# Kernel optimization log

Measured on AMD Instinct MI355X. Metric: run time of the kernel, lower is better.

The kernel has to match this reference:

```python
import jax, jax.numpy as jnp
import numpy as np
from jax import lax

LEVEL = 128  # level_num

def _bn(x, g, b, m, v):
    # inference-mode BatchNorm, channel axis = 1
    sh = (1, -1) + (1,) * (x.ndim - 2)
    return (x - m.reshape(sh)) * (g.reshape(sh) * lax.rsqrt(v.reshape(sh) + 1e-5)) + b.reshape(sh)

def _leaky(a):
    return jnp.where(a > 0, a, 0.01 * a)

def _l2n(a):
    return a / jnp.maximum(jnp.linalg.norm(a, axis=1, keepdims=True), 1e-12)

def _resize_bilinear_ac(x, oh, ow):
    # bilinear, align_corners=True, NCHW
    n, c, h, w = x.shape
    ys = jnp.linspace(0.0, h - 1.0, oh)
    xs = jnp.linspace(0.0, w - 1.0, ow)
    y0 = jnp.floor(ys).astype(jnp.int32)
    x0 = jnp.floor(xs).astype(jnp.int32)
    y1 = jnp.minimum(y0 + 1, h - 1)
    x1 = jnp.minimum(x0 + 1, w - 1)
    wy = (ys - y0)[:, None]
    wx = (xs - x0)[None, :]
    Y0, Y1, X0, X1 = y0[:, None], y1[:, None], x0[None, :], x1[None, :]
    return (x[:, :, Y0, X0] * (1 - wy) * (1 - wx) + x[:, :, Y0, X1] * (1 - wy) * wx
            + x[:, :, Y1, X0] * wy * (1 - wx) + x[:, :, Y1, X1] * wy * wx)

def _forward(x, conv1_w, bn1_g, bn1_b, bn1_m, bn1_v, conv2_w, f1_w, f2_w, f2_g, f2_b, f2_m, f2_v,
             out1_w, out1_g, out1_b, out1_m, out1_v, k_w, q_w, v_w, out_w, out_g, out_b, out_m, out_v):
    # conv1: 3x3 conv + BN + LeakyReLU
    y = lax.conv_general_dilated(x, conv1_w, (1, 1), 'SAME', dimension_numbers=('NCHW', 'OIHW', 'NCHW'))
    y = _leaky(_bn(y, bn1_g, bn1_b, bn1_m, bn1_v))
    # conv2: 1x1 conv, 256->128
    x2 = jnp.einsum('nchw,oc->nohw', y, conv2_w)
    N, C, H, W = x2.shape  # C = 128
    x_ave = x2.mean(axis=(2, 3), keepdims=True)  # [N,C,1,1]
    cos = (_l2n(x_ave) * _l2n(x2)).sum(1)        # [N,H,W]
    sh, sw = H // 3, W // 3
    L = sh * sw
    # H,W divisible by 3 -> adaptive_avg_pool2d is identity
    cs = cos.reshape(N, 3, sh, 3, sw).transpose(0, 1, 3, 2, 4).reshape(N, 9, L).transpose(0, 2, 1)  # [N,L,9]
    # LBP bit packing vs center (index 4); weight 0 at index 4 (strict > gives 0 there)
    bits = (cs > cs[:, :, 4:5]).astype(x.dtype)
    wts = jnp.array([1, 2, 4, 8, 0, 16, 32, 64, 128], dtype=x.dtype)
    code = (bits * wts).sum(-1)  # [N,L]
    mn = code.min(-1, keepdims=True)
    mx = code.max(-1, keepdims=True)
    code = (code - mn) / (mx - mn)
    cmin = code.min(-1, keepdims=True)
    cmax = code.max(-1, keepdims=True)
    qlv = (2 * jnp.arange(LEVEL, dtype=x.dtype) + 1) / (2 * LEVEL) * (cmax - cmin) + cmin  # [N,LEVEL]
    inter = (qlv[:, 1] - qlv[:, 0])[:, None, None]  # [N,1,1]
    quant = 1 - jnp.abs(qlv[:, None, :] - code[:, :, None])  # [N,L,LEVEL]
    quant = jnp.where(quant > 1 - inter, quant, 0.0)
    sta = quant.sum(1)                                       # [N,LEVEL]
    sta = sta / sta.sum(-1, keepdims=True)
    sta2 = jnp.stack([qlv, sta], axis=1)                     # [N,2,LEVEL]
    h1 = _leaky(jnp.einsum('ncl,oc->nol', sta2, f1_w))       # f1: 2->64
    h2 = jax.nn.relu(_bn(jnp.einsum('ncl,oc->nol', h1, f2_w), f2_g, f2_b, f2_m, f2_v))  # f2: 64->128
    xa = jnp.broadcast_to(x_ave[:, :, 0, 0][:, :, None], (N, C, LEVEL))
    s = jnp.concatenate([h2, xa], axis=1)                    # [N,256,LEVEL]
    s = jax.nn.relu(_bn(jnp.einsum('ncl,oc->nol', s, out1_w), out1_g, out1_b, out1_m, out1_v))
    k = jnp.einsum('ncl,oc->nol', s, k_w)
    q = jnp.einsum('ncl,oc->nol', s, q_w)
    v = jnp.einsum('ncl,oc->nol', s, v_w)
    w = jax.nn.softmax(jnp.einsum('ncl,ncm->nlm', k, q), axis=-1)  # bmm(k^T, q)
    f = jnp.einsum('nlm,ncm->ncl', w, v)                            # bmm(w, v^T) then transpose
    f = jax.nn.relu(_bn(jnp.einsum('ncl,oc->nol', f, out_w), out_g, out_b, out_m, out_v))
    out = jnp.einsum('ncl,npl->ncp', f, quant).reshape(N, 256, sh, sh)  # bmm(f, quant^T)
    return _resize_bilinear_ac(out, H, W)

def setup_inputs() -> dict:
    key = jax.random.key(0)
    ks = jax.random.split(key, 16)
    f32 = jnp.float32
    def nrm(k, shape, s=0.05):
        return s * jax.random.normal(k, shape, f32)
    def bnp(k, c):
        k1, k2, k3, k4 = jax.random.split(k, 4)
        return (1.0 + 0.1 * jax.random.normal(k1, (c,), f32),
                0.1 * jax.random.normal(k2, (c,), f32),
                0.1 * jax.random.normal(k3, (c,), f32),
                jax.random.uniform(k4, (c,), f32, 0.5, 1.5))
    d = {}
    d['x'] = jax.random.normal(ks[0], (32, 512, 48, 48), f32)
    d['conv1_w'] = nrm(ks[1], (256, 512, 3, 3))
    d['bn1_g'], d['bn1_b'], d['bn1_m'], d['bn1_v'] = bnp(ks[2], 256)
    d['conv2_w'] = nrm(ks[3], (128, 256))
    d['f1_w'] = nrm(ks[4], (64, 2), 0.3)
    d['f2_w'] = nrm(ks[5], (128, 64), 0.1)
    d['f2_g'], d['f2_b'], d['f2_m'], d['f2_v'] = bnp(ks[6], 128)
    d['out1_w'] = nrm(ks[7], (256, 256))
    d['out1_g'], d['out1_b'], d['out1_m'], d['out1_v'] = bnp(ks[8], 256)
    d['k_w'] = nrm(ks[9], (256, 256))
    d['q_w'] = nrm(ks[10], (256, 256))
    d['v_w'] = nrm(ks[11], (256, 256))
    d['out_w'] = nrm(ks[12], (256, 256))
    d['out_g'], d['out_b'], d['out_m'], d['out_v'] = bnp(ks[13], 256)
    return d

def reference(x, conv1_w, bn1_g, bn1_b, bn1_m, bn1_v, conv2_w, f1_w, f2_w, f2_g, f2_b, f2_m, f2_v,
              out1_w, out1_g, out1_b, out1_m, out1_v, k_w, q_w, v_w, out_w, out_g, out_b, out_m, out_v):
    return _forward(x, conv1_w, bn1_g, bn1_b, bn1_m, bn1_v, conv2_w, f1_w, f2_w, f2_g, f2_b, f2_m, f2_v,
                    out1_w, out1_g, out1_b, out1_m, out1_v, k_w, q_w, v_w, out_w, out_g, out_b, out_m, out_v)
```

## Files before the change

kernel.cpp:

```cpp
#include <hip/hip_runtime.h>
#include <math.h>

#define N_IMG 32
#define P2304 2304
#define CIN 512
#define CMID 256
#define C2 128
#define LEV 128

typedef _Float16 half8 __attribute__((ext_vector_type(8)));
typedef float f32x16 __attribute__((ext_vector_type(16)));
typedef unsigned short u16;
typedef unsigned int u32;

__device__ __forceinline__ float wredSum(float v){
#pragma unroll
  for (int o = 32; o > 0; o >>= 1) v += __shfl_down(v, o, 64);
  return v;
}
__device__ __forceinline__ float wredMax(float v){
#pragma unroll
  for (int o = 32; o > 0; o >>= 1) v = fmaxf(v, __shfl_down(v, o, 64));
  return v;
}
__device__ __forceinline__ float wredMin(float v){
#pragma unroll
  for (int o = 32; o > 0; o >>= 1) v = fminf(v, __shfl_down(v, o, 64));
  return v;
}

__device__ __forceinline__ void gll16(const void* g, void* l){
  __builtin_amdgcn_global_load_lds(
      (const __attribute__((address_space(1))) void*)g,
      (__attribute__((address_space(3))) void*)l, 16, 0, 0);
}

__global__ void prep_w1_kernel(const float* __restrict__ w1,
                               uint4* __restrict__ Wh, uint4* __restrict__ Wl){
  int fid = blockIdx.x * 256 + threadIdx.x;
  int lam = fid & 63;
  int c32 = (fid >> 6) & 3;
  int cot = (fid >> 8) & 1;
  int kt  = fid >> 9;
  int co = cot * 128 + c32 * 32 + (lam & 31);
  half8 vh, vl;
#pragma unroll
  for (int j = 0; j < 8; ++j){
    int k = kt * 16 + ((lam >> 5) << 3) + j;
    int r = k >> 9;
    int ci = k & 511;
    float v = w1[co * (CIN * 9) + ci * 9 + r];
    _Float16 h = (_Float16)v;
    vh[j] = h;
    vl[j] = (_Float16)((v - (float)h) * 2048.0f);
  }
  Wh[fid] = *(uint4*)&vh;
  Wl[fid] = *(uint4*)&vl;
}

__global__ void prep_w2_kernel(const float* __restrict__ w2,
                               uint4* __restrict__ Wh, uint4* __restrict__ Wl){
  int fid = blockIdx.x * 256 + threadIdx.x;
  int lam = fid & 63;
  int c32 = (fid >> 6) & 3;
  int kt  = fid >> 8;
  int co = c32 * 32 + (lam & 31);
  half8 vh, vl;
#pragma unroll
  for (int j = 0; j < 8; ++j){
    int k = kt * 16 + ((lam >> 5) << 3) + j;
    float v = w2[co * CMID + k];
    _Float16 h = (_Float16)v;
    vh[j] = h;
    vl[j] = (_Float16)((v - (float)h) * 2048.0f);
  }
  Wh[fid] = *(uint4*)&vh;
  Wl[fid] = *(uint4*)&vl;
}

__global__ void prep_bn_kernel(const float* __restrict__ g1, const float* __restrict__ b1,
                               const float* __restrict__ m1, const float* __restrict__ v1,
                               float* __restrict__ s1, float* __restrict__ t1){
  int c = threadIdx.x;
  float s = g1[c] * (1.0f / sqrtf(v1[c] + 1e-5f));
  s1[c] = s;
  t1[c] = b1[c] - m1[c] * s;
}

__global__ void prep_x_kernel(const float* __restrict__ x,
                              u16* __restrict__ xh, u16* __restrict__ xl,
                              int n0){
  __shared__ float tile[128 * 49];
  const int t = threadIdx.x;
  const int b = blockIdx.x;
  const int n_loc = b / 50;
  const int hp = b - n_loc * 50;
  const int n = n0 + n_loc;
  const int h = hp - 1;
  const bool vrow = (h >= 0) && (h < 48);
  const size_t orow = ((size_t)n_loc * 50 + hp) * 50 * 512;
  for (int cc = 0; cc < 4; ++cc){
    if (vrow){
      const float* src = x + (((size_t)n * 512 + cc * 128) * 48 + h) * 48;
#pragma unroll
      for (int i = 0; i < 24; ++i){
        int idx = t + 256 * i;
        int w = idx % 48;
        int c = idx / 48;
        tile[c * 49 + w] = src[(size_t)c * 2304 + w];
      }
    }
    __syncthreads();
    for (int i = 0; i < 13; ++i){
      int idx = t + 256 * i;
      if (idx < 3200){
        int cpair = idx & 63;
        int wp = idx >> 6;
        int w = wp - 1;
        float v0 = 0.f, v1 = 0.f;
        if (vrow && (unsigned)w < 48u){
          v0 = tile[(cpair * 2) * 49 + w];
          v1 = tile[(cpair * 2 + 1) * 49 + w];
        }
        _Float16 h0 = (_Float16)v0, h1 = (_Float16)v1;
        _Float16 l0 = (_Float16)((v0 - (float)h0) * 2048.0f);
        _Float16 l1 = (_Float16)((v1 - (float)h1) * 2048.0f);
        union { _Float16 hh[2]; u32 uu; } ph, pl;
        ph.hh[0] = h0; ph.hh[1] = h1;
        pl.hh[0] = l0; pl.hh[1] = l1;
        ((u32*)(xh + orow + (size_t)wp * 512 + cc * 128))[cpair] = ph.uu;
        ((u32*)(xl + orow + (size_t)wp * 512 + cc * 128))[cpair] = pl.uu;
      }
    }
    __syncthreads();
  }
}

#define COMPUTE_M(CUR, KF)                                                    \
  {                                                                           \
    const int ct0 = (g & 1) * 2, pt0 = (g >> 1) * 2;                          \
    half8 fAh[2], fAl[2], fBh[2], fBl[2];                                     \
    _Pragma("unroll")                                                         \
    for (int a = 0; a < 2; ++a){                                              \
      fAh[a] = *(half8*)&Abuf[CUR][KF][0][(ct0 + a) * 512 + lam * 8];         \
      fAl[a] = *(half8*)&Abuf[CUR][KF][1][(ct0 + a) * 512 + lam * 8];         \
      fBh[a] = *(half8*)&Bbuf[CUR][KF][0][(pt0 + a) * 512 + lam * 8];         \
      fBl[a] = *(half8*)&Bbuf[CUR][KF][1][(pt0 + a) * 512 + lam * 8];         \
    }                                                                         \
    _Pragma("unroll")                                                         \
    for (int a = 0; a < 2; ++a)                                               \
      _Pragma("unroll")                                                       \
      for (int b = 0; b < 2; ++b){                                            \
        acc_hh[a][b] = __builtin_amdgcn_mfma_f32_32x32x16_f16(                \
            fAh[a], fBh[b], acc_hh[a][b], 0, 0, 0);                           \
        acc_x[a][b] = __builtin_amdgcn_mfma_f32_32x32x16_f16(                 \
            fAh[a], fBl[b], acc_x[a][b], 0, 0, 0);                            \
        acc_x[a][b] = __builtin_amdgcn_mfma_f32_32x32x16_f16(                 \
            fAl[a], fBh[b], acc_x[a][b], 0, 0, 0);                            \
      }                                                                       \
  }

#define WAITV16 asm volatile("s_waitcnt vmcnt(16)" ::: "memory")
#define WAITV8  asm volatile("s_waitcnt vmcnt(8)"  ::: "memory")
#define WAITV0  asm volatile("s_waitcnt vmcnt(0)"  ::: "memory")
#define BARSB { __builtin_amdgcn_s_barrier(); __builtin_amdgcn_sched_barrier(0); }

template<int NC>
__global__ __launch_bounds__(256, 2) void conv1_lds_kernel(
    const u16* __restrict__ xh, const u16* __restrict__ xl,
    const uint4* __restrict__ Wh, const uint4* __restrict__ Wl,
    const float* __restrict__ s1, const float* __restrict__ t1,
    u16* __restrict__ yh, u16* __restrict__ yl, int n0)
{
  __shared__ _Float16 Abuf[4][2][2][2048];
  __shared__ _Float16 Bbuf[4][2][2][2048];
  const int t = threadIdx.x;
  const int lam = t & 63;
  const int g = t >> 6;

  const int xcd = blockIdx.x & 7;
  const int rest = blockIdx.x >> 3;
  const int NPX = NC / 8;
  const int n_loc = xcd * NPX + rest / 36;
  const int inner = rest % 36;
  const int pt_blk = inner % 18;
  const int cot = inner / 18;
  const int n = n0 + n_loc;

  const int pbase = pt_blk * 128;
  const int khi = lam >> 5;
  const int pp = (g << 5) + (lam & 31);
  const int p = pbase + pp;
  const int ph = p / 48, pw = p - ph * 48;
  const u16* xh_n = xh + (size_t)n_loc * 1280000;
  const u16* xl_n = xl + (size_t)n_loc * 1280000;

  const int S = 144;

  f32x16 acc_hh[2][2], acc_x[2][2];
#pragma unroll
  for (int a = 0; a < 2; ++a)
#pragma unroll
    for (int b = 0; b < 2; ++b){
#pragma unroll
      for (int e = 0; e < 16; ++e){ acc_hh[a][b][e] = 0.f; acc_x[a][b][e] = 0.f; }
    }

#define ISSUE1(SV, BUF)                                                       \
  {                                                                           \
    int s_ = (SV);                                                            \
    int k0_ = 2 * s_;                                                         \
    _Pragma("unroll")                                                         \
    for (int kf = 0; kf < 2; ++kf){                                           \
      int fg_ = ((k0_ + kf) * 2 + cot) * 4 + g;                               \
      gll16(Wh + fg_ * 64 + lam, &Abuf[BUF][kf][0][t * 8]);                   \
      gll16(Wl + fg_ * 64 + lam, &Abuf[BUF][kf][1][t * 8]);                   \
    }                                                                         \
    int r_ = k0_ >> 5;                                          \
    int cb_ = (k0_ & 31) << 4;                       \
    int hh_ = ph + r_ / 3;                                    \
    int ww_ = pw + r_ % 3;                                    \
    const u16* sh_ = xh_n + ((hh_ * 50 + ww_) << 9) + cb_ + (khi << 3);       \
    const u16* sl_ = xl_n + ((hh_ * 50 + ww_) << 9) + cb_ + (khi << 3);       \
    _Pragma("unroll")                                                         \
    for (int kf = 0; kf < 2; ++kf){                                           \
      gll16(sh_ + kf * 16, &Bbuf[BUF][kf][0][t * 8]);                         \
      gll16(sl_ + kf * 16, &Bbuf[BUF][kf][1][t * 8]);                         \
    }                                                                         \
  }

  ISSUE1(0, 0);
  ISSUE1(1, 1);

  for (int s = 0; s < S - 2; ++s){
    ISSUE1(s + 2, (s + 2) & 3);
    WAITV16;
    BARSB;
    __builtin_amdgcn_s_setprio(1);
    COMPUTE_M(s & 3, 0);
    COMPUTE_M(s & 3, 1);
    __builtin_amdgcn_s_setprio(0);
  }
  WAITV8;
  BARSB;
  __builtin_amdgcn_s_setprio(1);
  COMPUTE_M((S - 2) & 3, 0);
  COMPUTE_M((S - 2) & 3, 1);
  __builtin_amdgcn_s_setprio(0);
  WAITV0;
  BARSB;
  __builtin_amdgcn_s_setprio(1);
  COMPUTE_M((S - 1) & 3, 0);
  COMPUTE_M((S - 1) & 3, 1);
  __builtin_amdgcn_s_setprio(0);
#undef ISSUE1

  const int cobase = cot * 128;
#pragma unroll
  for (int a = 0; a < 2; ++a){
    const int ctile = (g & 1) * 2 + a;
#pragma unroll
    for (int b = 0; b < 2; ++b){
      const int ptile = (g >> 1) * 2 + b;
      const int pg = pbase + ptile * 32 + (lam & 31);
      u16* dh = yh + (((size_t)n * P2304 + pg) << 8);
      u16* dl = yl + (((size_t)n * P2304 + pg) << 8);
#pragma unroll
      for (int q = 0; q < 4; ++q){
        const int co0 = cobase + ctile * 32 + 8 * q + 4 * khi;
        union { _Float16 h[4]; uint2 u; } Uh, Ul;
#pragma unroll
        for (int i = 0; i < 4; ++i){
          const int rg = 4 * q + i;
          const int co = co0 + i;
          float val = acc_hh[a][b][rg] + acc_x[a][b][rg] * (1.0f / 2048.0f);
          val = val * s1[co] + t1[co];
          val = val > 0.f ? val : 0.01f * val;
          _Float16 h = (_Float16)val;
          Uh.h[i] = h;
          Ul.h[i] = (_Float16)((val - (float)h) * 2048.0f);
        }
        *(uint2*)(dh + co0) = Uh.u;
        *(uint2*)(dl + co0) = Ul.u;
      }
    }
  }
}

__global__ __launch_bounds__(256, 2) void conv2_lds_kernel(
    const u16* __restrict__ yh, const u16* __restrict__ yl,
    const uint4* __restrict__ Wh, const uint4* __restrict__ Wl,
    float* __restrict__ out)
{
  __shared__ _Float16 Abuf[4][2][2][2048];
  __shared__ _Float16 Bbuf[4][2][2][2048];
  const int t = threadIdx.x;
  const int lam = t & 63;
  const int g = t >> 6;

  const int pt_blk = blockIdx.x % 18;
  const int n = blockIdx.x / 18;
  const int pbase = pt_blk * 128;
  const int khi = lam >> 5;
  const int p = pbase + (g << 5) + (lam & 31);
  const u16* yh_n = yh + (size_t)n * P2304 * 256;
  const u16* yl_n = yl + (size_t)n * P2304 * 256;

  const int S = 8;

  f32x16 acc_hh[2][2], acc_x[2][2];
#pragma unroll
  for (int a = 0; a < 2; ++a)
#pragma unroll
    for (int b = 0; b < 2; ++b){
#pragma unroll
      for (int e = 0; e < 16; ++e){ acc_hh[a][b][e] = 0.f; acc_x[a][b][e] = 0.f; }
    }

#define ISSUE2(SV, BUF)                                                       \
  {                                                                           \
    int s_ = (SV);                                                            \
    _Pragma("unroll")                                                         \
    for (int kf = 0; kf < 2; ++kf){                                           \
      int fg_ = (2 * s_ + kf) * 4 + g;                                        \
      gll16(Wh + fg_ * 64 + lam, &Abuf[BUF][kf][0][t * 8]);                   \
      gll16(Wl + fg_ * 64 + lam, &Abuf[BUF][kf][1][t * 8]);                   \
    }                                                                         \
    const u16* sh_ = yh_n + ((size_t)p << 8) + (s_ << 5) + (khi << 3);        \
    const u16* sl_ = yl_n + ((size_t)p << 8) + (s_ << 5) + (khi << 3);        \
    _Pragma("unroll")                                                         \
    for (int kf = 0; kf < 2; ++kf){                                           \
      gll16(sh_ + kf * 16, &Bbuf[BUF][kf][0][t * 8]);                         \
      gll16(sl_ + kf * 16, &Bbuf[BUF][kf][1][t * 8]);                         \
    }                                                                         \
  }

  ISSUE2(0, 0);
  ISSUE2(1, 1);

  for (int s = 0; s < S - 2; ++s){
    ISSUE2(s + 2, (s + 2) & 3);
    WAITV16;
    BARSB;
    __builtin_amdgcn_s_setprio(1);
    COMPUTE_M(s & 3, 0);
    COMPUTE_M(s & 3, 1);
    __builtin_amdgcn_s_setprio(0);
  }
  WAITV8;
  BARSB;
  __builtin_amdgcn_s_setprio(1);
  COMPUTE_M((S - 2) & 3, 0);
  COMPUTE_M((S - 2) & 3, 1);
  __builtin_amdgcn_s_setprio(0);
  WAITV0;
  BARSB;
  __builtin_amdgcn_s_setprio(1);
  COMPUTE_M((S - 1) & 3, 0);
  COMPUTE_M((S - 1) & 3, 1);
  __builtin_amdgcn_s_setprio(0);
#undef ISSUE2

#pragma unroll
  for (int a = 0; a < 2; ++a){
    const int ctile = (g & 1) * 2 + a;
#pragma unroll
    for (int b = 0; b < 2; ++b){
      const int ptile = (g >> 1) * 2 + b;
      const int pg = pbase + ptile * 32 + (lam & 31);
#pragma unroll
      for (int rg = 0; rg < 16; ++rg){
        const int row = (rg & 3) + 8 * (rg >> 2) + 4 * khi;
        const int co = ctile * 32 + row;
        float val = acc_hh[a][b][rg] + acc_x[a][b][rg] * (1.0f / 2048.0f);
        out[((size_t)n * C2 + co) * P2304 + pg] = val;
      }
    }
  }
}

template<int R, int CPT, int COTN, bool BN>
__global__ __launch_bounds__(256, 2) void conv_mfma_kernel(
    const float* __restrict__ in, const uint4* __restrict__ Wh, const uint4* __restrict__ Wl,
    const float* __restrict__ s1, const float* __restrict__ t1, float* __restrict__ out)
{
  __shared__ _Float16 Abuf[2][2][2][2048];
  __shared__ _Float16 Bbuf[2][2][2][2048];
  const int t = threadIdx.x;
  const int lam = t & 63;
  const int g = t >> 6;

  int n, pt_blk, cot;
  if (COTN == 2){
    int xcd = blockIdx.x & 7;
    int rest = blockIdx.x >> 3;
    n = xcd * 4 + rest / 36;
    int inner = rest % 36;
    pt_blk = inner % 18;
    cot = inner / 18;
  } else {
    pt_blk = blockIdx.x % 18;
    cot = 0;
    n = blockIdx.x / 18;
  }
  const int pbase = pt_blk * 128;
  const int cobase = cot * 128;

  const int khi = lam >> 5;
  const int pp = (g << 5) + (lam & 31);
  const int p = pbase + pp;
  const int ph = p / 48, pw = p - ph * 48;
  const float* in_n = in + (size_t)n * CPT * P2304;

  const int S = (R * CPT) / 32;
  const int KTPT = CPT / 16;

  f32x16 acc_hh[2][2], acc_x[2][2];
#pragma unroll
  for (int a = 0; a < 2; ++a)
#pragma unroll
    for (int b = 0; b < 2; ++b){
#pragma unroll
      for (int e = 0; e < 16; ++e){ acc_hh[a][b][e] = 0.f; acc_x[a][b][e] = 0.f; }
    }

  uint4 rAh[2], rAl[2];
  float rB[16];
  bool vmask;

#define ISSUE(SV)                                                             \
  {                                                                           \
    int s_ = (SV);                                                            \
    _Pragma("unroll")                                                         \
    for (int kf = 0; kf < 2; ++kf){                                           \
      int fi = (((2 * s_ + kf) * COTN + cot) * 4 + g) * 64 + lam;             \
      rAh[kf] = Wh[fi];                                                       \
      rAl[kf] = Wl[fi];                                                       \
    }                                                                         \
    int r_ = (R == 1) ? 0 : ((2 * s_) / KTPT);                                \
    int cbase_ = ((2 * s_) % KTPT) * 16;                                      \
    int dh_ = (R == 1) ? 0 : (r_ / 3 - 1);                                    \
    int dw_ = (R == 1) ? 0 : (r_ - (r_ / 3) * 3 - 1);                         \
    int hh_ = ph + dh_, ww_ = pw + dw_;                                       \
    vmask = ((unsigned)hh_ < 48u) & ((unsigned)ww_ < 48u);                    \
    int hc_ = min(max(hh_, 0), 47), wc_ = min(max(ww_, 0), 47);               \
    const float* src_ = in_n + hc_ * 48 + wc_                                 \
                        + (size_t)(cbase_ + khi * 8) * P2304;                 \
    _Pragma("unroll")                                                         \
    for (int kf = 0; kf < 2; ++kf)                                            \
      _Pragma("unroll")                                                       \
      for (int j = 0; j < 8; ++j)                                             \
        rB[kf * 8 + j] = src_[(kf * 16 + j) * P2304];                         \
  }

#define STASH(NXT)                                                            \
  {                                                                           \
    _Pragma("unroll")                                                         \
    for (int kf = 0; kf < 2; ++kf){                                           \
      *(uint4*)&Abuf[NXT][kf][0][t * 8] = rAh[kf];                            \
      *(uint4*)&Abuf[NXT][kf][1][t * 8] = rAl[kf];                            \
      half8 vh, vl;                                                           \
      _Pragma("unroll")                                                       \
      for (int j = 0; j < 8; ++j){                                            \
        float v = vmask ? rB[kf * 8 + j] : 0.0f;                              \
        _Float16 h = (_Float16)v;                                             \
        vh[j] = h;                                                            \
        vl[j] = (_Float16)((v - (float)h) * 2048.0f);                        \
      }                                                                       \
      *(half8*)&Bbuf[NXT][kf][0][t * 8] = vh;                                 \
      *(half8*)&Bbuf[NXT][kf][1][t * 8] = vl;                                 \
    }                                                                         \
  }

  ISSUE(0);
  STASH(0);
  __syncthreads();

  for (int s = 0; s < S; ++s){
    const int cur = s & 1, nxt = cur ^ 1;
    const bool more = (s + 1 < S);
    if (more) ISSUE(s + 1);
    COMPUTE_M(cur, 0);
    if (more) STASH(nxt);
    COMPUTE_M(cur, 1);
    __syncthreads();
  }
#undef ISSUE
#undef STASH

  const int M = COTN * 128;
#pragma unroll
  for (int a = 0; a < 2; ++a){
    const int ctile = (g & 1) * 2 + a;
#pragma unroll
    for (int b = 0; b < 2; ++b){
      const int ptile = (g >> 1) * 2 + b;
      const int pg = pbase + ptile * 32 + (lam & 31);
#pragma unroll
      for (int rg = 0; rg < 16; ++rg){
        const int row = (rg & 3) + 8 * (rg >> 2) + 4 * (lam >> 5);
        const int co = cobase + ctile * 32 + row;
        float val = acc_hh[a][b][rg] + acc_x[a][b][rg] * (1.0f / 2048.0f);
        if (BN){
          val = val * s1[co] + t1[co];
          val = val > 0.f ? val : 0.01f * val;
        }
        out[((size_t)n * M + co) * P2304 + pg] = val;
      }
    }
  }
}

__global__ void xave_kernel(const float* __restrict__ x2, float* __restrict__ xave){
  __shared__ float red[4];
  int nc = blockIdx.x, t = threadIdx.x;
  const float* row = x2 + nc * P2304;
  float s = 0.f;
#pragma unroll
  for (int i = 0; i < 9; i++) s += row[t + 256 * i];
  float w = wredSum(s);
  if ((t & 63) == 0) red[t >> 6] = w;
  __syncthreads();
  if (t == 0) xave[nc] = (red[0] + red[1] + red[2] + red[3]) * (1.0f / 2304.0f);
}

__global__ void xan_kernel(const float* __restrict__ xave, float* __restrict__ xan){
  __shared__ float red[2];
  int n = blockIdx.x, t = threadIdx.x;
  float v = xave[n * 128 + t];
  float w = wredSum(v * v);
  if ((t & 63) == 0) red[t >> 6] = w;
  __syncthreads();
  float norm = fmaxf(sqrtf(red[0] + red[1]), 1e-12f);
  xan[n * 128 + t] = v / norm;
}

__global__ void cos_kernel(const float* __restrict__ x2, const float* __restrict__ xan,
                           float* __restrict__ cosb){
  int idx = blockIdx.x * 256 + threadIdx.x;
  if (idx >= N_IMG * P2304) return;
  int n = idx / P2304;
  int p = idx - n * P2304;
  const float* xp = x2 + n * C2 * P2304 + p;
  const float* an = xan + n * 128;
  float dot = 0.f, ss = 0.f;
  for (int c = 0; c < 128; c++){
    float v = xp[c * P2304];
    dot += an[c] * v;
    ss  += v * v;
  }
  cosb[idx] = dot / fmaxf(sqrtf(ss), 1e-12f);
}

__global__ void lbp_kernel(const float* __restrict__ cosb, float* __restrict__ code,
                           float* __restrict__ qlv){
  __shared__ float red[4];
  int n = blockIdx.x;
  int l = threadIdx.x;
  int ir = l >> 4, ic = l & 15;
  const float* cn = cosb + n * P2304;
  float cs4 = cn[(16 + ir) * 48 + (16 + ic)];
  const float wts[9] = {1.f, 2.f, 4.f, 8.f, 0.f, 16.f, 32.f, 64.f, 128.f};
  float codev = 0.f;
#pragma unroll
  for (int j = 0; j < 9; j++){
    int jr = j / 3, jc = j - 3 * (j / 3);
    float vv = cn[(jr * 16 + ir) * 48 + (jc * 16 + ic)];
    if (vv > cs4) codev += wts[j];
  }
  float w;
  w = wredMin(codev);
  if ((l & 63) == 0) red[l >> 6] = w;
  __syncthreads();
  float mn = fminf(fminf(red[0], red[1]), fminf(red[2], red[3]));
  __syncthreads();
  w = wredMax(codev);
  if ((l & 63) == 0) red[l >> 6] = w;
  __syncthreads();
  float mx = fmaxf(fmaxf(red[0], red[1]), fmaxf(red[2], red[3]));
  __syncthreads();
  float cd = (codev - mn) / (mx - mn);
  w = wredMin(cd);
  if ((l & 63) == 0) red[l >> 6] = w;
  __syncthreads();
  float cmin = fminf(fminf(red[0], red[1]), fminf(red[2], red[3]));
  __syncthreads();
  w = wredMax(cd);
  if ((l & 63) == 0) red[l >> 6] = w;
  __syncthreads();
  float cmax = fmaxf(fmaxf(red[0], red[1]), fmaxf(red[2], red[3]));
  code[n * 256 + l] = cd;
  if (l < 128){
    float tmp = (float)(2 * l + 1) * (1.0f / 256.0f);
    qlv[n * 128 + l] = tmp * (cmax - cmin) + cmin;
  }
}

__global__ void quant_kernel(const float* __restrict__ code, const float* __restrict__ qlv,
                             float* __restrict__ quantT){
  __shared__ float cs[256];
  __shared__ float qs[128];
  int n = blockIdx.x, t = threadIdx.x;
  cs[t] = code[n * 256 + t];
  if (t < 128) qs[t] = qlv[n * 128 + t];
  __syncthreads();
  float thr = 1.0f - (qs[1] - qs[0]);
  float* dst = quantT + n * LEV * 256;
#pragma unroll 4
  for (int i = 0; i < 128; i++){
    int v = t + 256 * i;
    int lv = v >> 8;
    int p = v & 255;
    float qq = 1.0f - fabsf(qs[lv] - cs[p]);
    dst[v] = (qq > thr) ? qq : 0.f;
  }
}

__global__ void sta_kernel(const float* __restrict__ quantT, float* __restrict__ sta){
  __shared__ float red[2];
  int n = blockIdx.x, i = threadIdx.x;
  const float* qr = quantT + (n * LEV + i) * 256;
  float s = 0.f;
  for (int p = 0; p < 256; p++) s += qr[p];
  float w = wredSum(s);
  if ((i & 63) == 0) red[i >> 6] = w;
  __syncthreads();
  float tot = red[0] + red[1];
  sta[n * 128 + i] = s / tot;
}

__global__ void h1_kernel(const float* __restrict__ f1w, const float* __restrict__ qlv,
                          const float* __restrict__ sta, float* __restrict__ h1){
  int idx = blockIdx.x * 256 + threadIdx.x;
  if (idx >= N_IMG * 64 * 128) return;
  int l = idx & 127;
  int n = idx >> 13;
  int o = (idx >> 7) & 63;
  float a = f1w[o * 2] * qlv[n * 128 + l] + f1w[o * 2 + 1] * sta[n * 128 + l];
  h1[idx] = a > 0.f ? a : 0.01f * a;
}

__global__ void gemm_w_kernel(const float* __restrict__ Wm, const float* __restrict__ B,
                              float* __restrict__ Cout, int Cdim, int O, int total, int mode,
                              const float* __restrict__ g, const float* __restrict__ bb,
                              const float* __restrict__ mm, const float* __restrict__ vv){
  int idx = blockIdx.x * 256 + threadIdx.x;
  if (idx >= total) return;
  int per_n = (O >> 2) << 7;
  int n = idx / per_n;
  int rem = idx - n * per_n;
  int o0 = (rem >> 7) << 2;
  int l = rem & 127;
  const float* Bn = B + (n * Cdim) * 128 + l;
  const float* w0 = Wm + (o0 + 0) * Cdim;
  const float* w1 = Wm + (o0 + 1) * Cdim;
  const float* w2 = Wm + (o0 + 2) * Cdim;
  const float* w3 = Wm + (o0 + 3) * Cdim;
  float a0 = 0, a1 = 0, a2 = 0, a3 = 0;
  for (int c = 0; c < Cdim; c++){
    float bv = Bn[c * 128];
    a0 += w0[c] * bv; a1 += w1[c] * bv; a2 += w2[c] * bv; a3 += w3[c] * bv;
  }
  float av[4] = {a0, a1, a2, a3};
#pragma unroll
  for (int j = 0; j < 4; j++){
    int o = o0 + j;
    float val = av[j];
    if (mode == 1){
      float s = g[o] * (1.0f / sqrtf(vv[o] + 1e-5f));
      val = (val - mm[o]) * s + bb[o];
      val = fmaxf(val, 0.f);
    }
    Cout[(n * O + o) * 128 + l] = val;
  }
}

__global__ void concat_kernel(const float* __restrict__ h2, const float* __restrict__ xave,
                              float* __restrict__ s){
  int idx = blockIdx.x * 256 + threadIdx.x;
  if (idx >= N_IMG * 256 * 128) return;
  int l = idx & 127;
  int c = (idx >> 7) & 255;
  int n = idx >> 15;
  s[idx] = (c < 128) ? h2[(n * 128 + c) * 128 + l] : xave[n * 128 + (c - 128)];
}

__global__ void attn_sc_kernel(const float* __restrict__ k, const float* __restrict__ q,
                               float* __restrict__ sc){
  int idx = blockIdx.x * 256 + threadIdx.x;
  if (idx >= N_IMG * 32 * 128) return;
  int m = idx & 127;
  int l0 = ((idx >> 7) & 31) << 2;
  int n = idx >> 12;
  const float* kn = k + n * 256 * 128;
  const float* qn = q + n * 256 * 128 + m;
  float a0 = 0, a1 = 0, a2 = 0, a3 = 0;
  for (int c = 0; c < 256; c++){
    float qv = qn[c * 128];
    const float* kr = kn + c * 128 + l0;
    a0 += kr[0] * qv; a1 += kr[1] * qv; a2 += kr[2] * qv; a3 += kr[3] * qv;
  }
  float* dst = sc + (n * 128 + l0) * 128 + m;
  dst[0] = a0; dst[128] = a1; dst[256] = a2; dst[384] = a3;
}

__global__ void softmax_kernel(float* __restrict__ sc){
  __shared__ float red[2];
  int row = blockIdx.x;
  int t = threadIdx.x;
  float v = sc[row * 128 + t];
  float w = wredMax(v);
  if ((t & 63) == 0) red[t >> 6] = w;
  __syncthreads();
  float mx = fmaxf(red[0], red[1]);
  float e = expf(v - mx);
  float s = wredSum(e);
  __syncthreads();
  if ((t & 63) == 0) red[t >> 6] = s;
  __syncthreads();
  sc[row * 128 + t] = e / (red[0] + red[1]);
}

__global__ void transpose_sc_kernel(const float* __restrict__ sc, float* __restrict__ scT){
  int idx = blockIdx.x * 256 + threadIdx.x;
  if (idx >= N_IMG * 128 * 128) return;
  int l = idx & 127;
  int m = (idx >> 7) & 127;
  int n = idx >> 14;
  scT[idx] = sc[(n * 128 + l) * 128 + m];
}

__global__ void attn_f_kernel(const float* __restrict__ vb, const float* __restrict__ scT,
                              float* __restrict__ f){
  int idx = blockIdx.x * 256 + threadIdx.x;
  if (idx >= N_IMG * 64 * 128) return;
  int l = idx & 127;
  int c0 = ((idx >> 7) & 63) << 2;
  int n = idx >> 13;
  const float* vn = vb + (n * 256 + c0) * 128;
  const float* sn = scT + n * 128 * 128 + l;
  float a0 = 0, a1 = 0, a2 = 0, a3 = 0;
  for (int m = 0; m < 128; m++){
    float sv = sn[m * 128];
    a0 += vn[m] * sv; a1 += vn[128 + m] * sv; a2 += vn[256 + m] * sv; a3 += vn[384 + m] * sv;
  }
  float* dst = f + (n * 256 + c0) * 128 + l;
  dst[0] = a0; dst[128] = a1; dst[256] = a2; dst[384] = a3;
}

__global__ void final_kernel(const float* __restrict__ g, const float* __restrict__ quantT,
                             float* __restrict__ outs){
  int idx = blockIdx.x * 256 + threadIdx.x;
  if (idx >= N_IMG * 64 * 256) return;
  int p = idx & 255;
  int c0 = ((idx >> 8) & 63) << 2;
  int n = idx >> 14;
  const float* gn = g + (n * 256 + c0) * 128;
  const float* qn = quantT + (n * LEV) * 256 + p;
  float a0 = 0, a1 = 0, a2 = 0, a3 = 0;
  for (int lv = 0; lv < 128; lv++){
    float qv = qn[lv * 256];
    a0 += gn[lv] * qv; a1 += gn[128 + lv] * qv; a2 += gn[256 + lv] * qv; a3 += gn[384 + lv] * qv;
  }
  float* dst = outs + (n * 256 + c0) * 256 + p;
  dst[0] = a0; dst[256] = a1; dst[512] = a2; dst[768] = a3;
}

__global__ void resize_kernel(const float* __restrict__ outs, float* __restrict__ dout){
  int idx = blockIdx.x * 256 + threadIdx.x;
  if (idx >= N_IMG * 256 * P2304) return;
  int ow = idx % 48;
  int tmp = idx / 48;
  int oh = tmp % 48;
  int nc = tmp / 48;
  const float* src = outs + nc * 256;
  float fy = oh * (15.0f / 47.0f);
  float fx = ow * (15.0f / 47.0f);
  int y0 = (int)fy;
  int x0 = (int)fx;
  int y1 = min(y0 + 1, 15);
  int x1 = min(x0 + 1, 15);
  float wy = fy - (float)y0;
  float wx = fx - (float)x0;
  float v00 = src[y0 * 16 + x0], v01 = src[y0 * 16 + x1];
  float v10 = src[y1 * 16 + x0], v11 = src[y1 * 16 + x1];
  dout[idx] = v00 * (1.f - wy) * (1.f - wx) + v01 * (1.f - wy) * wx
            + v10 * wy * (1.f - wx) + v11 * wy * wx;
}

extern "C" void kernel_launch(void* const* d_in, const int* in_sizes, int n_in,
                              void* d_out, int out_size, void* d_ws, size_t ws_size,
                              hipStream_t stream)
{
  const float* x       = (const float*)d_in[0];
  const float* conv1_w = (const float*)d_in[1];
  const float* bn1_g   = (const float*)d_in[2];
  const float* bn1_b   = (const float*)d_in[3];
  const float* bn1_m   = (const float*)d_in[4];
  const float* bn1_v   = (const float*)d_in[5];
  const float* conv2_w = (const float*)d_in[6];
  const float* f1_w    = (const float*)d_in[7];
  const float* f2_w    = (const float*)d_in[8];
  const float* f2_g    = (const float*)d_in[9];
  const float* f2_b    = (const float*)d_in[10];
  const float* f2_m    = (const float*)d_in[11];
  const float* f2_v    = (const float*)d_in[12];
  const float* out1_w  = (const float*)d_in[13];
  const float* out1_g  = (const float*)d_in[14];
  const float* out1_b  = (const float*)d_in[15];
  const float* out1_m  = (const float*)d_in[16];
  const float* out1_v  = (const float*)d_in[17];
  const float* k_w     = (const float*)d_in[18];
  const float* q_w     = (const float*)d_in[19];
  const float* v_w     = (const float*)d_in[20];
  const float* out_w   = (const float*)d_in[21];
  const float* out_g   = (const float*)d_in[22];
  const float* out_b   = (const float*)d_in[23];
  const float* out_m   = (const float*)d_in[24];
  const float* out_v   = (const float*)d_in[25];

  float* ws = (float*)d_ws;
  float* dout = (float*)d_out;

  float* w_y   = ws;
  float* w_x2  = ws + 18874368;
  float* w_W1h = ws + 28311552;
  float* w_W1l = ws + 28901376;
  float* w_W2h = ws + 29491200;
  float* w_W2l = ws + 29507584;
  float* w_s1  = ws + 29523968;
  float* w_t1  = ws + 29524224;
  float* w_xave = w_y + 0;
  float* w_xan  = w_y + 4096;
  float* w_cos  = w_y + 8192;
  float* w_code = w_y + 81920;
  float* w_qlv  = w_y + 90112;
  float* w_sta  = w_y + 94208;
  float* w_quant= w_y + 98304;
  float* w_h1   = w_y + 1146880;
  float* w_h2   = w_y + 1409024;
  float* w_s    = w_y + 1933312;
  float* w_k    = w_y + 2981888;
  float* w_q    = w_y + 4030464;
  float* w_v    = w_y + 5079040;
  float* w_sc   = w_y + 6127616;
  float* w_scT  = w_y + 6651904;
  float* w_f    = w_y + 7176192;
  float* w_g    = w_y + 8224768;
  float* w_outs = w_y + 9273344;
  float* w_s2   = w_y + 11370496;

  prep_w1_kernel<<<576, 256, 0, stream>>>(conv1_w, (uint4*)w_W1h, (uint4*)w_W1l);
  prep_w2_kernel<<<16, 256, 0, stream>>>(conv2_w, (uint4*)w_W2h, (uint4*)w_W2l);
  prep_bn_kernel<<<1, 256, 0, stream>>>(bn1_g, bn1_b, bn1_m, bn1_v, w_s1, w_t1);

  const size_t BASE_F = 29524480;
  const size_t XPI_F  = 640000;
  const size_t ws_f = ws_size / 4;
  int NCc = 0;
  if (ws_f >= BASE_F + 2 * 32 * XPI_F)      NCc = 32;
  else if (ws_f >= BASE_F + 2 * 16 * XPI_F) NCc = 16;

  if (NCc > 0){
    u16* w_xh = (u16*)(ws + BASE_F);
    u16* w_xl = w_xh + (size_t)NCc * 1280000;
    u16* w_yh = (u16*)w_y;
    u16* w_yl = (u16*)(w_y + 9437184);
    const int nchunk = N_IMG / NCc;
    for (int c = 0; c < nchunk; ++c){
      int n0 = c * NCc;
      prep_x_kernel<<<NCc * 50, 256, 0, stream>>>(x, w_xh, w_xl, n0);
      if (NCc == 32)
        conv1_lds_kernel<32><<<1152, 256, 0, stream>>>(
            w_xh, w_xl, (const uint4*)w_W1h, (const uint4*)w_W1l, w_s1, w_t1,
            w_yh, w_yl, n0);
      else
        conv1_lds_kernel<16><<<576, 256, 0, stream>>>(
            w_xh, w_xl, (const uint4*)w_W1h, (const uint4*)w_W1l, w_s1, w_t1,
            w_yh, w_yl, n0);
    }
    conv2_lds_kernel<<<576, 256, 0, stream>>>(
        w_yh, w_yl, (const uint4*)w_W2h, (const uint4*)w_W2l, w_x2);
  } else {
    conv_mfma_kernel<9, 512, 2, true><<<1152, 256, 0, stream>>>(
        x, (const uint4*)w_W1h, (const uint4*)w_W1l, w_s1, w_t1, w_y);
    conv_mfma_kernel<1, 256, 1, false><<<576, 256, 0, stream>>>(
        w_y, (const uint4*)w_W2h, (const uint4*)w_W2l, w_s1, w_t1, w_x2);
  }

  xave_kernel<<<4096, 256, 0, stream>>>(w_x2, w_xave);
  xan_kernel<<<32, 128, 0, stream>>>(w_xave, w_xan);
  cos_kernel<<<288, 256, 0, stream>>>(w_x2, w_xan, w_cos);
  lbp_kernel<<<32, 256, 0, stream>>>(w_cos, w_code, w_qlv);
  quant_kernel<<<32, 256, 0, stream>>>(w_code, w_qlv, w_quant);
  sta_kernel<<<32, 128, 0, stream>>>(w_quant, w_sta);
  h1_kernel<<<1024, 256, 0, stream>>>(f1_w, w_qlv, w_sta, w_h1);
  gemm_w_kernel<<<512, 256, 0, stream>>>(f2_w, w_h1, w_h2, 64, 128, N_IMG * 32 * 128, 1,
                                         f2_g, f2_b, f2_m, f2_v);
  concat_kernel<<<4096, 256, 0, stream>>>(w_h2, w_xave, w_s);
  gemm_w_kernel<<<1024, 256, 0, stream>>>(out1_w, w_s, w_s2, 256, 256, N_IMG * 64 * 128, 1,
                                          out1_g, out1_b, out1_m, out1_v);
  gemm_w_kernel<<<1024, 256, 0, stream>>>(k_w, w_s2, w_k, 256, 256, N_IMG * 64 * 128, 0,
                                          nullptr, nullptr, nullptr, nullptr);
  gemm_w_kernel<<<1024, 256, 0, stream>>>(q_w, w_s2, w_q, 256, 256, N_IMG * 64 * 128, 0,
                                          nullptr, nullptr, nullptr, nullptr);
  gemm_w_kernel<<<1024, 256, 0, stream>>>(v_w, w_s2, w_v, 256, 256, N_IMG * 64 * 128, 0,
                                          nullptr, nullptr, nullptr, nullptr);
  attn_sc_kernel<<<512, 256, 0, stream>>>(w_k, w_q, w_sc);
  softmax_kernel<<<4096, 128, 0, stream>>>(w_sc);
  transpose_sc_kernel<<<2048, 256, 0, stream>>>(w_sc, w_scT);
  attn_f_kernel<<<1024, 256, 0, stream>>>(w_v, w_scT, w_f);
  gemm_w_kernel<<<1024, 256, 0, stream>>>(out_w, w_f, w_g, 256, 256, N_IMG * 64 * 128, 1,
                                          out_g, out_b, out_m, out_v);
  final_kernel<<<2048, 256, 0, stream>>>(w_g, w_quant, w_outs);
  resize_kernel<<<73728, 256, 0, stream>>>(w_outs, dout);
}
```

Measured before the change: 1.774 ms.

## Use channel-blocked 16-wide layout for padded input and conv1 output; double-buffer LDS

Changes the fp16 hi/lo staging layout of the padded input and of the conv1 activations from pixel-major with 512/256 contiguous channels to a channel-block-major layout with 16 channels per block. The conv1 and conv2 LDS pipelines drop from 4-deep to 2-deep buffering, and each refill is issued after an extra barrier once the current stage is consumed. Halving LDS may allow more resident blocks per CU, but the two-stage pipeline exposes more load latency and adds a barrier per step. The new layout also changes global access strides for the gather loads and the epilogue stores.

```diff
diff --git a/kernel.cpp b/kernel.cpp
--- a/kernel.cpp
+++ b/kernel.cpp
@@ -98,7 +98,7 @@
   const int n = n0 + n_loc;
   const int h = hp - 1;
   const bool vrow = (h >= 0) && (h < 48);
-  const size_t orow = ((size_t)n_loc * 50 + hp) * 50 * 512;
+  const size_t base_n = (size_t)n_loc * 1280000;
   for (int cc = 0; cc < 4; ++cc){
     if (vrow){
       const float* src = x + (((size_t)n * 512 + cc * 128) * 48 + h) * 48;
@@ -114,13 +114,16 @@
     for (int i = 0; i < 13; ++i){
       int idx = t + 256 * i;
       if (idx < 3200){
-        int cpair = idx & 63;
-        int wp = idx >> 6;
+        int ck_loc = idx / 400;
+        int rem = idx - ck_loc * 400;
+        int wp = rem >> 3;
+        int clp = rem & 7;
         int w = wp - 1;
+        int c_loc = ck_loc * 16 + clp * 2;
         float v0 = 0.f, v1 = 0.f;
         if (vrow && (unsigned)w < 48u){
-          v0 = tile[(cpair * 2) * 49 + w];
-          v1 = tile[(cpair * 2 + 1) * 49 + w];
+          v0 = tile[c_loc * 49 + w];
+          v1 = tile[(c_loc + 1) * 49 + w];
         }
         _Float16 h0 = (_Float16)v0, h1 = (_Float16)v1;
         _Float16 l0 = (_Float16)((v0 - (float)h0) * 2048.0f);
@@ -128,8 +131,10 @@
         union { _Float16 hh[2]; u32 uu; } ph, pl;
         ph.hh[0] = h0; ph.hh[1] = h1;
         pl.hh[0] = l0; pl.hh[1] = l1;
-        ((u32*)(xh + orow + (size_t)wp * 512 + cc * 128))[cpair] = ph.uu;
-        ((u32*)(xl + orow + (size_t)wp * 512 + cc * 128))[cpair] = pl.uu;
+        size_t off = base_n + ((size_t)(cc * 8 + ck_loc) * 2500
+                               + hp * 50 + wp) * 16 + clp * 2;
+        *(u32*)(xh + off) = ph.uu;
+        *(u32*)(xl + off) = pl.uu;
       }
     }
     __syncthreads();
@@ -160,7 +165,6 @@
       }                                                                       \
   }
 
-#define WAITV16 asm volatile("s_waitcnt vmcnt(16)" ::: "memory")
 #define WAITV8  asm volatile("s_waitcnt vmcnt(8)"  ::: "memory")
 #define WAITV0  asm volatile("s_waitcnt vmcnt(0)"  ::: "memory")
 #define BARSB { __builtin_amdgcn_s_barrier(); __builtin_amdgcn_sched_barrier(0); }
@@ -172,8 +176,8 @@
     const float* __restrict__ s1, const float* __restrict__ t1,
     u16* __restrict__ yh, u16* __restrict__ yl, int n0)
 {
-  __shared__ _Float16 Abuf[4][2][2][2048];
-  __shared__ _Float16 Bbuf[4][2][2][2048];
+  __shared__ _Float16 Abuf[2][2][2][2048];
+  __shared__ _Float16 Bbuf[2][2][2][2048];
   const int t = threadIdx.x;
   const int lam = t & 63;
   const int g = t >> 6;
@@ -217,41 +221,36 @@
       gll16(Wl + fg_ * 64 + lam, &Abuf[BUF][kf][1][t * 8]);                   \
     }                                                                         \
     int r_ = k0_ >> 5;                                          \
-    int cb_ = (k0_ & 31) << 4;                       \
-    int hh_ = ph + r_ / 3;                                    \
-    int ww_ = pw + r_ % 3;                                    \
-    const u16* sh_ = xh_n + ((hh_ * 50 + ww_) << 9) + cb_ + (khi << 3);       \
-    const u16* sl_ = xl_n + ((hh_ * 50 + ww_) << 9) + cb_ + (khi << 3);       \
+    int ck0_ = k0_ & 31;                         \
+    int qpp_ = (ph + r_ / 3) * 50 + (pw + r_ % 3);            \
     _Pragma("unroll")                                                         \
     for (int kf = 0; kf < 2; ++kf){                                           \
-      gll16(sh_ + kf * 16, &Bbuf[BUF][kf][0][t * 8]);                         \
-      gll16(sl_ + kf * 16, &Bbuf[BUF][kf][1][t * 8]);                         \
+      size_t o_ = ((size_t)(ck0_ + kf) * 2500 + qpp_) * 16 + (khi << 3);      \
+      gll16(xh_n + o_, &Bbuf[BUF][kf][0][t * 8]);                             \
+      gll16(xl_n + o_, &Bbuf[BUF][kf][1][t * 8]);                             \
     }                                                                         \
   }
 
   ISSUE1(0, 0);
   ISSUE1(1, 1);
 
-  for (int s = 0; s < S - 2; ++s){
-    ISSUE1(s + 2, (s + 2) & 3);
-    WAITV16;
+  for (int s = 0; s < S - 1; ++s){
+    WAITV8;
     BARSB;
     __builtin_amdgcn_s_setprio(1);
-    COMPUTE_M(s & 3, 0);
-    COMPUTE_M(s & 3, 1);
+    COMPUTE_M(s & 1, 0);
+    COMPUTE_M(s & 1, 1);
     __builtin_amdgcn_s_setprio(0);
-  }
-  WAITV8;
-  BARSB;
-  __builtin_amdgcn_s_setprio(1);
-  COMPUTE_M((S - 2) & 3, 0);
-  COMPUTE_M((S - 2) & 3, 1);
-  __builtin_amdgcn_s_setprio(0);
+    if (s + 2 < S){
+      BARSB;
+      ISSUE1(s + 2, s & 1);
+    }
+  }
   WAITV0;
   BARSB;
   __builtin_amdgcn_s_setprio(1);
-  COMPUTE_M((S - 1) & 3, 0);
-  COMPUTE_M((S - 1) & 3, 1);
+  COMPUTE_M((S - 1) & 1, 0);
+  COMPUTE_M((S - 1) & 1, 1);
   __builtin_amdgcn_s_setprio(0);
 #undef ISSUE1
 
@@ -263,11 +262,10 @@
     for (int b = 0; b < 2; ++b){
       const int ptile = (g >> 1) * 2 + b;
       const int pg = pbase + ptile * 32 + (lam & 31);
-      u16* dh = yh + (((size_t)n * P2304 + pg) << 8);
-      u16* dl = yl + (((size_t)n * P2304 + pg) << 8);
 #pragma unroll
       for (int q = 0; q < 4; ++q){
         const int co0 = cobase + ctile * 32 + 8 * q + 4 * khi;
+        const int co16 = co0 >> 4, col = co0 & 15;
         union { _Float16 h[4]; uint2 u; } Uh, Ul;
 #pragma unroll
         for (int i = 0; i < 4; ++i){
@@ -280,8 +278,9 @@
           Uh.h[i] = h;
           Ul.h[i] = (_Float16)((val - (float)h) * 2048.0f);
         }
-        *(uint2*)(dh + co0) = Uh.u;
-        *(uint2*)(dl + co0) = Ul.u;
+        size_t off = (((size_t)n * 16 + co16) * P2304 + pg) * 16 + col;
+        *(uint2*)(yh + off) = Uh.u;
+        *(uint2*)(yl + off) = Ul.u;
       }
     }
   }
@@ -292,8 +291,8 @@
     const uint4* __restrict__ Wh, const uint4* __restrict__ Wl,
     float* __restrict__ out)
 {
-  __shared__ _Float16 Abuf[4][2][2][2048];
-  __shared__ _Float16 Bbuf[4][2][2][2048];
+  __shared__ _Float16 Abuf[2][2][2][2048];
+  __shared__ _Float16 Bbuf[2][2][2][2048];
   const int t = threadIdx.x;
   const int lam = t & 63;
   const int g = t >> 6;
@@ -303,8 +302,8 @@
   const int pbase = pt_blk * 128;
   const int khi = lam >> 5;
   const int p = pbase + (g << 5) + (lam & 31);
-  const u16* yh_n = yh + (size_t)n * P2304 * 256;
-  const u16* yl_n = yl + (size_t)n * P2304 * 256;
+  const u16* yh_n = yh + (size_t)n * 589824;
+  const u16* yl_n = yl + (size_t)n * 589824;
 
   const int S = 8;
 
@@ -320,44 +319,41 @@
 #define ISSUE2(SV, BUF)                                                       \
   {                                                                           \
     int s_ = (SV);                                                            \
+    int k0_ = 2 * s_;                                                         \
     _Pragma("unroll")                                                         \
     for (int kf = 0; kf < 2; ++kf){                                           \
-      int fg_ = (2 * s_ + kf) * 4 + g;                                        \
+      int fg_ = (k0_ + kf) * 4 + g;                                           \
       gll16(Wh + fg_ * 64 + lam, &Abuf[BUF][kf][0][t * 8]);                   \
       gll16(Wl + fg_ * 64 + lam, &Abuf[BUF][kf][1][t * 8]);                   \
     }                                                                         \
-    const u16* sh_ = yh_n + ((size_t)p << 8) + (s_ << 5) + (khi << 3);        \
-    const u16* sl_ = yl_n + ((size_t)p << 8) + (s_ << 5) + (khi << 3);        \
     _Pragma("unroll")                                                         \
     for (int kf = 0; kf < 2; ++kf){                                           \
-      gll16(sh_ + kf * 16, &Bbuf[BUF][kf][0][t * 8]);                         \
-      gll16(sl_ + kf * 16, &Bbuf[BUF][kf][1][t * 8]);                         \
+      size_t o_ = ((size_t)(k0_ + kf) * P2304 + p) * 16 + (khi << 3);         \
+      gll16(yh_n + o_, &Bbuf[BUF][kf][0][t * 8]);                             \
+      gll16(yl_n + o_, &Bbuf[BUF][kf][1][t * 8]);                             \
     }                                                                         \
   }
 
   ISSUE2(0, 0);
   ISSUE2(1, 1);
 
-  for (int s = 0; s < S - 2; ++s){
-    ISSUE2(s + 2, (s + 2) & 3);
-    WAITV16;
+  for (int s = 0; s < S - 1; ++s){
+    WAITV8;
     BARSB;
     __builtin_amdgcn_s_setprio(1);
-    COMPUTE_M(s & 3, 0);
-    COMPUTE_M(s & 3, 1);
+    COMPUTE_M(s & 1, 0);
+    COMPUTE_M(s & 1, 1);
     __builtin_amdgcn_s_setprio(0);
-  }
-  WAITV8;
-  BARSB;
-  __builtin_amdgcn_s_setprio(1);
-  COMPUTE_M((S - 2) & 3, 0);
-  COMPUTE_M((S - 2) & 3, 1);
-  __builtin_amdgcn_s_setprio(0);
+    if (s + 2 < S){
+      BARSB;
+      ISSUE2(s + 2, s & 1);
+    }
+  }
   WAITV0;
   BARSB;
   __builtin_amdgcn_s_setprio(1);
-  COMPUTE_M((S - 1) & 3, 0);
-  COMPUTE_M((S - 1) & 3, 1);
+  COMPUTE_M((S - 1) & 1, 0);
+  COMPUTE_M((S - 1) & 1, 1);
   __builtin_amdgcn_s_setprio(0);
 #undef ISSUE2
 
@@ -465,7 +461,7 @@
         float v = vmask ? rB[kf * 8 + j] : 0.0f;                              \
         _Float16 h = (_Float16)v;                                             \
         vh[j] = h;                                                            \
-        vl[j] = (_Float16)((v - (float)h) * 2048.0f);                        \
+        vl[j] = (_Float16)((v - (float)h) * 2048.0f);                         \
       }                                                                       \
       *(half8*)&Bbuf[NXT][kf][0][t * 8] = vh;                                 \
       *(half8*)&Bbuf[NXT][kf][1][t * 8] = vl;                                 \
```

New measurement: 1.624 ms. 8.4% less time.
